# Kernel optimization log

Measured on AMD Instinct MI355X. Metric: run time of the kernel, lower is better.

The kernel has to match this reference:

```python
import jax, jax.numpy as jnp
import numpy as np

EPS = 1e-9
# i = 7,6,...,-1 use exp_factor = -(4**i); i = -2 uses 0.0 (matches torch's reversed(range(-2,8)))
EXP_FACTORS = np.array([-(4.0 ** i) for i in range(7, -2, -1)] + [0.0], dtype=np.float32)


def setup_inputs() -> dict:
    key = jax.random.key(0)
    k1, k2 = jax.random.split(key)
    B, N, D = 16, 2048, 3
    preds = jax.random.normal(k1, (B, N, D), dtype=jnp.float32)
    labels = jax.random.normal(k2, (B, N, D), dtype=jnp.float32)
    return {"preds": preds, "labels": labels}


def _pairwise_dist(p1, p2):
    # ||p1||^2 + ||p2||^2 - 2 p1 . p2  -> [B, N, N]
    p1n = jnp.sum(p1 * p1, axis=-1)[..., :, None]
    p2n = jnp.sum(p2 * p2, axis=-1)[..., None, :]
    return p1n + p2n - 2.0 * jnp.einsum('bnd,bmd->bnm', p1, p2)


def _approx_match(pwdist):
    B, N, _ = pwdist.shape
    match0 = jnp.zeros_like(pwdist)
    cost0 = jnp.ones((B, 1, N), dtype=pwdist.dtype)      # per-target remaining capacity
    curr0 = jnp.ones((B, N, 1), dtype=pwdist.dtype)      # per-source remaining currency

    def step(carry, ef):
        match, cost, currency = carry
        bids = jnp.exp(ef * pwdist) * cost
        bids = bids * currency / (jnp.sum(bids, axis=1, keepdims=True) + EPS)
        bid_wt = jnp.minimum(cost / (jnp.sum(bids, axis=1, keepdims=True) + EPS), 1.0)
        bids = bids * bid_wt
        match = match + bids
        cost = jnp.maximum(cost - jnp.sum(bids, axis=1, keepdims=True), 0.0)
        currency = jnp.maximum(currency - jnp.sum(bids, axis=2, keepdims=True), 0.0)
        return (match, cost, currency), None

    (match, _, _), _ = jax.lax.scan(step, (match0, cost0, curr0), jnp.asarray(EXP_FACTORS))
    return match


def reference(preds, labels):
    pwdist = _pairwise_dist(preds, labels)
    match = _approx_match(pwdist)
    return jnp.sum(match * pwdist)
```

## Files before the change

### kernel.cpp

```cpp
#include <hip/hip_runtime.h>
#include <cstddef>

#define BB    16
#define NN    2048
#define BN    (BB * NN)
#define EPSF  1e-9f
#define TPB   512
#define CPT   2
#define SPLIT 16
#define TILE  128
#define CHUNK 1024

extern "C" __device__ float __ocml_native_exp2_f32(float);
__device__ __forceinline__ float fast_exp2(float x) {
#if __has_builtin(__builtin_amdgcn_exp2f)
    return __builtin_amdgcn_exp2f(x);
#else
    return __ocml_native_exp2_f32(x);
#endif
}

__global__ __launch_bounds__(TPB, 4) void passA(
    const float* __restrict__ preds, const float* __restrict__ labels,
    const float* __restrict__ curprev, float* __restrict__ curout,
    const float* __restrict__ RSprev, const float* __restrict__ RRprev,
    float* __restrict__ RSz, float* __restrict__ RRz,
    float* __restrict__ Sacc, float* __restrict__ Tacc,
    float* __restrict__ out, float c1, int k)
{
    __shared__ float4 s_p[TILE];
    __shared__ float  s_cu[TILE];
    __shared__ float  s_red[2];
    int blk = blockIdx.x;
    int split = blk & 15, mc = (blk >> 4) & 1, b = blk >> 5;
    int t = threadIdx.x;
    int base = b * NN;

    if (t < TILE) {
        int idx = base + split * TILE + t;
        const float* p = preds + (size_t)idx * 3;
        float px = p[0], py = p[1], pz = p[2];
        float pn = px * px + py * py + pz * pz;
        float cu, contrib = 0.0f;
        if (k == 0) cu = 1.0f;
        else {
            float cup = curprev[idx], rs = RSprev[idx], rr = RRprev[idx];
            contrib = cup * rr;
            cu = fmaxf(cup * (1.0f - rs), 0.0f);
        }
        s_p[t]  = make_float4(px, py, pz, c1 * pn);
        s_cu[t] = cu;
        if (mc == 0) {
            curout[idx] = cu;
            RSz[idx] = 0.0f; RRz[idx] = 0.0f;
        }
        if (k > 0 && mc == 0) {
#pragma unroll
            for (int o = 32; o > 0; o >>= 1) contrib += __shfl_down(contrib, o, 64);
            if ((t & 63) == 0) s_red[t >> 6] = contrib;
        }
    }

    int m0 = mc * CHUNK + t;
    float gx[CPT], gy[CPT], gz[CPT], am[CPT], Sa[CPT], Ta[CPT];
    float n2c1 = -2.0f * c1;
#pragma unroll
    for (int c = 0; c < CPT; c++) {
        int m = m0 + c * TPB;
        const float* l = labels + (size_t)(base + m) * 3;
        float lx = l[0], ly = l[1], lz = l[2];
        gx[c] = n2c1 * lx; gy[c] = n2c1 * ly; gz[c] = n2c1 * lz;
        am[c] = c1 * (lx * lx + ly * ly + lz * lz);
        Sa[c] = 0.0f; Ta[c] = 0.0f;
    }
    __syncthreads();
    if (k > 0 && mc == 0 && t == 0) atomicAdd(out, s_red[0] + s_red[1]);

#pragma unroll 8
    for (int j = 0; j < TILE; j++) {
        float4 P = s_p[j]; float cu = s_cu[j];
#pragma unroll
        for (int c = 0; c < CPT; c++) {
            float arg = fmaf(P.x, gx[c], fmaf(P.y, gy[c], fmaf(P.z, gz[c], P.w + am[c])));
            float e = fast_exp2(arg);
            Sa[c] += e;
            Ta[c] = fmaf(e, cu, Ta[c]);
        }
    }
#pragma unroll
    for (int c = 0; c < CPT; c++) {
        int idx = base + m0 + c * TPB;
        atomicAdd(&Sacc[idx], Sa[c]);
        atomicAdd(&Tacc[idx], Ta[c]);
    }
}

__global__ __launch_bounds__(TPB, 4) void passB(
    const float* __restrict__ preds, const float* __restrict__ labels,
    const float* __restrict__ Sread, const float* __restrict__ Tread,
    const float* __restrict__ costprev, float* __restrict__ costout,
    float* __restrict__ Sz, float* __restrict__ Tz,
    float* __restrict__ RSacc, float* __restrict__ RRacc,
    float c1, float invc1, int k, int last)
{
    __shared__ float4 s_l[TILE];
    __shared__ float  s_cc[TILE];
    int blk = blockIdx.x;
    int split = blk & 15, nc = (blk >> 4) & 1, b = blk >> 5;
    int t = threadIdx.x;
    int base = b * NN;

    if (t < TILE) {
        int idx = base + split * TILE + t;
        const float* l = labels + (size_t)idx * 3;
        float lx = l[0], ly = l[1], lz = l[2];
        float lm2 = lx * lx + ly * ly + lz * lz;
        float S = Sread[idx], T = Tread[idx];
        float cost = (k == 0) ? 1.0f : costprev[idx];
        float D1 = fmaf(cost, S, EPSF);
        float S2 = cost * T / D1;
        float bw = fminf(cost / (S2 + EPSF), 1.0f);
        float cc = cost * bw / D1;
        if (nc == 0) {
            costout[idx] = fmaxf(fmaf(-S2, bw, cost), 0.0f);
            Sz[idx] = 0.0f; Tz[idx] = 0.0f;
        }
        if (last) s_l[t] = make_float4(lx, ly, lz, lm2);
        else      s_l[t] = make_float4(-2.0f * c1 * lx, -2.0f * c1 * ly,
                                       -2.0f * c1 * lz, c1 * lm2);
        s_cc[t] = cc;
    }

    int n0 = nc * CHUNK + t;
    float px[CPT], py[CPT], pz[CPT], qq[CPT], RSa[CPT], RRa[CPT];
#pragma unroll
    for (int c = 0; c < CPT; c++) {
        int n = n0 + c * TPB;
        const float* p = preds + (size_t)(base + n) * 3;
        px[c] = p[0]; py[c] = p[1]; pz[c] = p[2];
        float pn = px[c] * px[c] + py[c] * py[c] + pz[c] * pz[c];
        qq[c] = last ? pn : c1 * pn;
        RSa[c] = 0.0f; RRa[c] = 0.0f;
    }
    __syncthreads();

    if (!last) {
#pragma unroll 8
        for (int j = 0; j < TILE; j++) {
            float4 L = s_l[j]; float ccj = s_cc[j];
#pragma unroll
            for (int c = 0; c < CPT; c++) {
                float arg = fmaf(px[c], L.x, fmaf(py[c], L.y, fmaf(pz[c], L.z, qq[c] + L.w)));
                float e = fast_exp2(arg);
                float w = e * ccj;
                RSa[c] += w;
                RRa[c] = fmaf(w, arg, RRa[c]);
            }
        }
#pragma unroll
        for (int c = 0; c < CPT; c++) {
            int idx = base + n0 + c * TPB;
            atomicAdd(&RSacc[idx], RSa[c]);
            atomicAdd(&RRacc[idx], RRa[c] * invc1);
        }
    } else {
#pragma unroll 8
        for (int j = 0; j < TILE; j++) {
            float4 L = s_l[j]; float ccj = s_cc[j];
#pragma unroll
            for (int c = 0; c < CPT; c++) {
                float dot = fmaf(px[c], L.x, fmaf(py[c], L.y, pz[c] * L.z));
                float pw  = fmaf(-2.0f, dot, qq[c] + L.w);
                RRa[c] = fmaf(ccj, pw, RRa[c]);
            }
        }
#pragma unroll
        for (int c = 0; c < CPT; c++) {
            int idx = base + n0 + c * TPB;
            atomicAdd(&RRacc[idx], RRa[c]);
        }
    }
}

__global__ void finalK(const float* __restrict__ cur, const float* __restrict__ RR,
                       float* __restrict__ out)
{
    int t = threadIdx.x;
    int i = blockIdx.x * TPB + t;
    float contrib = cur[i] * RR[i];
#pragma unroll
    for (int o = 32; o > 0; o >>= 1) contrib += __shfl_down(contrib, o, 64);
    __shared__ float s_red[TPB / 64];
    if ((t & 63) == 0) s_red[t >> 6] = contrib;
    __syncthreads();
    if (t == 0) {
        float s = 0.0f;
#pragma unroll
        for (int w = 0; w < TPB / 64; w++) s += s_red[w];
        atomicAdd(out, s);
    }
}

extern "C" void kernel_launch(void* const* d_in, const int* in_sizes, int n_in,
                              void* d_out, int out_size, void* d_ws, size_t ws_size,
                              hipStream_t stream) {
    const float* preds  = (const float*)d_in[0];
    const float* labels = (const float*)d_in[1];
    float* out = (float*)d_out;
    float* ws  = (float*)d_ws;

    float* S[2]     = {ws + 0 * BN, ws + 2 * BN};
    float* T[2]     = {ws + 1 * BN, ws + 3 * BN};
    float* RS[2]    = {ws + 4 * BN, ws + 6 * BN};
    float* RR[2]    = {ws + 5 * BN, ws + 7 * BN};
    float* curb[2]  = {ws + 8 * BN, ws + 9 * BN};
    float* costb[2] = {ws + 10 * BN, ws + 11 * BN};

    hipMemsetAsync(d_out, 0, sizeof(float), stream);
    hipMemsetAsync(ws, 0, (size_t)2 * BN * sizeof(float), stream);

    static const float efs[10] = {-16384.0f, -4096.0f, -1024.0f, -256.0f, -64.0f,
                                  -16.0f, -4.0f, -1.0f, -0.25f, 0.0f};
    const float log2e = 1.44269504088896f;
    for (int k = 0; k < 10; k++) {
        float c1 = efs[k] * log2e;
        float invc1 = (efs[k] != 0.0f) ? 1.0f / c1 : 0.0f;
        int pk = k & 1, pp = (k + 1) & 1;
        passA<<<512, TPB, 0, stream>>>(preds, labels,
            curb[pp], curb[pk],
            RS[pp], RR[pp],
            RS[pk], RR[pk],
            S[pk], T[pk],
            out, c1, k);
        passB<<<512, TPB, 0, stream>>>(preds, labels,
            S[pk], T[pk],
            costb[pk], costb[pp],
            S[pp], T[pp],
            RS[pk], RR[pk],
            c1, invc1, k, (k == 9) ? 1 : 0);
    }
    finalK<<<BN / TPB, TPB, 0, stream>>>(curb[1], RR[1], out);
}
```

Baseline: 350.0 us.

## Collapse final auction step algebraically, skip underflowed exps, retile passes

The last iteration has exp factor zero, so every bid weight is constant. That step is now computed in closed form by a per-batch kernel using moment sums of the labels (count, squared norms, coordinate sums) instead of an N×N pass. For the three sharpest early iterations, wavefront-uniform checks skip exp2 work when every lane's argument is below the float underflow point. Tiling also changes: each block covers all 2048 columns with 4 per thread and 64-row tiles, and the per-row factors are read from shared memory as float4. These are algebraically exact, but the skip relies on exp2 flushing to zero, and the moment-based sum may round differently.

```diff
diff --git a/kernel.cpp b/kernel.cpp
--- a/kernel.cpp
+++ b/kernel.cpp
@@ -6,10 +6,10 @@
 #define BN    (BB * NN)
 #define EPSF  1e-9f
 #define TPB   512
-#define CPT   2
-#define SPLIT 16
-#define TILE  128
-#define CHUNK 1024
+#define CPT   4
+#define SPLIT 32
+#define TILE  64
+#define UFLO  -151.0f
 
 extern "C" __device__ float __ocml_native_exp2_f32(float);
 __device__ __forceinline__ float fast_exp2(float x) {
@@ -20,6 +20,23 @@
 #endif
 }
 
+__device__ __forceinline__ float f4c(float4 v, int u) {
+    return (u == 0) ? v.x : ((u == 1) ? v.y : ((u == 2) ? v.z : v.w));
+}
+
+__device__ __forceinline__ float block_sum(float v, int t, float* tmp8) {
+#pragma unroll
+    for (int o = 32; o > 0; o >>= 1) v += __shfl_down(v, o, 64);
+    __syncthreads();
+    if ((t & 63) == 0) tmp8[t >> 6] = v;
+    __syncthreads();
+    float s = 0.0f;
+#pragma unroll
+    for (int w = 0; w < TPB / 64; w++) s += tmp8[w];
+    return s;
+}
+
+template<int SKIP>
 __global__ __launch_bounds__(TPB, 4) void passA(
     const float* __restrict__ preds, const float* __restrict__ labels,
     const float* __restrict__ curprev, float* __restrict__ curout,
@@ -29,10 +46,10 @@
     float* __restrict__ out, float c1, int k)
 {
     __shared__ float4 s_p[TILE];
-    __shared__ float  s_cu[TILE];
-    __shared__ float  s_red[2];
+    __shared__ float4 s_cu4[TILE / 4];
+    __shared__ float  s_red;
     int blk = blockIdx.x;
-    int split = blk & 15, mc = (blk >> 4) & 1, b = blk >> 5;
+    int split = blk & (SPLIT - 1), b = blk >> 5;
     int t = threadIdx.x;
     int base = b * NN;
 
@@ -48,65 +65,75 @@
             contrib = cup * rr;
             cu = fmaxf(cup * (1.0f - rs), 0.0f);
         }
-        s_p[t]  = make_float4(px, py, pz, c1 * pn);
-        s_cu[t] = cu;
-        if (mc == 0) {
-            curout[idx] = cu;
-            RSz[idx] = 0.0f; RRz[idx] = 0.0f;
-        }
-        if (k > 0 && mc == 0) {
+        s_p[t] = make_float4(px, py, pz, c1 * pn);
+        ((float*)s_cu4)[t] = cu;
+        curout[idx] = cu;
+        RSz[idx] = 0.0f; RRz[idx] = 0.0f;
+        if (k > 0) {
 #pragma unroll
             for (int o = 32; o > 0; o >>= 1) contrib += __shfl_down(contrib, o, 64);
-            if ((t & 63) == 0) s_red[t >> 6] = contrib;
-        }
-    }
-
-    int m0 = mc * CHUNK + t;
+            if (t == 0) s_red = contrib;
+        }
+    }
+
     float gx[CPT], gy[CPT], gz[CPT], am[CPT], Sa[CPT], Ta[CPT];
     float n2c1 = -2.0f * c1;
 #pragma unroll
     for (int c = 0; c < CPT; c++) {
-        int m = m0 + c * TPB;
-        const float* l = labels + (size_t)(base + m) * 3;
+        const float* l = labels + (size_t)(base + t + c * TPB) * 3;
         float lx = l[0], ly = l[1], lz = l[2];
         gx[c] = n2c1 * lx; gy[c] = n2c1 * ly; gz[c] = n2c1 * lz;
         am[c] = c1 * (lx * lx + ly * ly + lz * lz);
         Sa[c] = 0.0f; Ta[c] = 0.0f;
     }
     __syncthreads();
-    if (k > 0 && mc == 0 && t == 0) atomicAdd(out, s_red[0] + s_red[1]);
-
-#pragma unroll 8
-    for (int j = 0; j < TILE; j++) {
-        float4 P = s_p[j]; float cu = s_cu[j];
-#pragma unroll
-        for (int c = 0; c < CPT; c++) {
-            float arg = fmaf(P.x, gx[c], fmaf(P.y, gy[c], fmaf(P.z, gz[c], P.w + am[c])));
-            float e = fast_exp2(arg);
-            Sa[c] += e;
-            Ta[c] = fmaf(e, cu, Ta[c]);
-        }
-    }
-#pragma unroll
-    for (int c = 0; c < CPT; c++) {
-        int idx = base + m0 + c * TPB;
+    if (k > 0 && t == 0) atomicAdd(out, s_red);
+
+#pragma unroll 2
+    for (int j4 = 0; j4 < TILE / 4; j4++) {
+        float4 cu4 = s_cu4[j4];
+#pragma unroll
+        for (int u = 0; u < 4; u++) {
+            float4 P = s_p[j4 * 4 + u];
+            float cu = f4c(cu4, u);
+#pragma unroll
+            for (int c = 0; c < CPT; c++) {
+                float arg = fmaf(P.x, gx[c], fmaf(P.y, gy[c], fmaf(P.z, gz[c], P.w + am[c])));
+                if constexpr (SKIP) {
+                    if (__any(arg > UFLO)) {
+                        float e = fast_exp2(arg);
+                        Sa[c] += e;
+                        Ta[c] = fmaf(e, cu, Ta[c]);
+                    }
+                } else {
+                    float e = fast_exp2(arg);
+                    Sa[c] += e;
+                    Ta[c] = fmaf(e, cu, Ta[c]);
+                }
+            }
+        }
+    }
+#pragma unroll
+    for (int c = 0; c < CPT; c++) {
+        int idx = base + t + c * TPB;
         atomicAdd(&Sacc[idx], Sa[c]);
         atomicAdd(&Tacc[idx], Ta[c]);
     }
 }
 
+template<int SKIP>
 __global__ __launch_bounds__(TPB, 4) void passB(
     const float* __restrict__ preds, const float* __restrict__ labels,
     const float* __restrict__ Sread, const float* __restrict__ Tread,
     const float* __restrict__ costprev, float* __restrict__ costout,
     float* __restrict__ Sz, float* __restrict__ Tz,
     float* __restrict__ RSacc, float* __restrict__ RRacc,
-    float c1, float invc1, int k, int last)
+    float c1, float invc1, int k)
 {
     __shared__ float4 s_l[TILE];
-    __shared__ float  s_cc[TILE];
+    __shared__ float4 s_cc4[TILE / 4];
     int blk = blockIdx.x;
-    int split = blk & 15, nc = (blk >> 4) & 1, b = blk >> 5;
+    int split = blk & (SPLIT - 1), b = blk >> 5;
     int t = threadIdx.x;
     int base = b * NN;
 
@@ -121,84 +148,113 @@
         float S2 = cost * T / D1;
         float bw = fminf(cost / (S2 + EPSF), 1.0f);
         float cc = cost * bw / D1;
-        if (nc == 0) {
-            costout[idx] = fmaxf(fmaf(-S2, bw, cost), 0.0f);
-            Sz[idx] = 0.0f; Tz[idx] = 0.0f;
-        }
-        if (last) s_l[t] = make_float4(lx, ly, lz, lm2);
-        else      s_l[t] = make_float4(-2.0f * c1 * lx, -2.0f * c1 * ly,
-                                       -2.0f * c1 * lz, c1 * lm2);
-        s_cc[t] = cc;
-    }
-
-    int n0 = nc * CHUNK + t;
+        costout[idx] = fmaxf(fmaf(-S2, bw, cost), 0.0f);
+        Sz[idx] = 0.0f; Tz[idx] = 0.0f;
+        s_l[t] = make_float4(-2.0f * c1 * lx, -2.0f * c1 * ly,
+                             -2.0f * c1 * lz, c1 * lm2);
+        ((float*)s_cc4)[t] = cc;
+    }
+
     float px[CPT], py[CPT], pz[CPT], qq[CPT], RSa[CPT], RRa[CPT];
 #pragma unroll
     for (int c = 0; c < CPT; c++) {
-        int n = n0 + c * TPB;
-        const float* p = preds + (size_t)(base + n) * 3;
+        const float* p = preds + (size_t)(base + t + c * TPB) * 3;
         px[c] = p[0]; py[c] = p[1]; pz[c] = p[2];
-        float pn = px[c] * px[c] + py[c] * py[c] + pz[c] * pz[c];
-        qq[c] = last ? pn : c1 * pn;
+        qq[c] = c1 * (px[c] * px[c] + py[c] * py[c] + pz[c] * pz[c]);
         RSa[c] = 0.0f; RRa[c] = 0.0f;
     }
     __syncthreads();
 
-    if (!last) {
-#pragma unroll 8
-        for (int j = 0; j < TILE; j++) {
-            float4 L = s_l[j]; float ccj = s_cc[j];
+#pragma unroll 2
+    for (int j4 = 0; j4 < TILE / 4; j4++) {
+        float4 cc4 = s_cc4[j4];
+#pragma unroll
+        for (int u = 0; u < 4; u++) {
+            float4 L = s_l[j4 * 4 + u];
+            float ccj = f4c(cc4, u);
 #pragma unroll
             for (int c = 0; c < CPT; c++) {
                 float arg = fmaf(px[c], L.x, fmaf(py[c], L.y, fmaf(pz[c], L.z, qq[c] + L.w)));
-                float e = fast_exp2(arg);
-                float w = e * ccj;
-                RSa[c] += w;
-                RRa[c] = fmaf(w, arg, RRa[c]);
+                if constexpr (SKIP) {
+                    if (__any(arg > UFLO)) {
+                        float e = fast_exp2(arg);
+                        float w = e * ccj;
+                        RSa[c] += w;
+                        RRa[c] = fmaf(w, arg, RRa[c]);
+                    }
+                } else {
+                    float e = fast_exp2(arg);
+                    float w = e * ccj;
+                    RSa[c] += w;
+                    RRa[c] = fmaf(w, arg, RRa[c]);
+                }
             }
         }
-#pragma unroll
-        for (int c = 0; c < CPT; c++) {
-            int idx = base + n0 + c * TPB;
-            atomicAdd(&RSacc[idx], RSa[c]);
-            atomicAdd(&RRacc[idx], RRa[c] * invc1);
-        }
-    } else {
-#pragma unroll 8
-        for (int j = 0; j < TILE; j++) {
-            float4 L = s_l[j]; float ccj = s_cc[j];
-#pragma unroll
-            for (int c = 0; c < CPT; c++) {
-                float dot = fmaf(px[c], L.x, fmaf(py[c], L.y, pz[c] * L.z));
-                float pw  = fmaf(-2.0f, dot, qq[c] + L.w);
-                RRa[c] = fmaf(ccj, pw, RRa[c]);
-            }
-        }
-#pragma unroll
-        for (int c = 0; c < CPT; c++) {
-            int idx = base + n0 + c * TPB;
-            atomicAdd(&RRacc[idx], RRa[c]);
-        }
-    }
-}
-
-__global__ void finalK(const float* __restrict__ cur, const float* __restrict__ RR,
-                       float* __restrict__ out)
+    }
+#pragma unroll
+    for (int c = 0; c < CPT; c++) {
+        int idx = base + t + c * TPB;
+        atomicAdd(&RSacc[idx], RSa[c]);
+        atomicAdd(&RRacc[idx], RRa[c] * invc1);
+    }
+}
+
+__global__ __launch_bounds__(TPB, 1) void k9(
+    const float* __restrict__ preds, const float* __restrict__ labels,
+    const float* __restrict__ cur8, const float* __restrict__ RS8,
+    const float* __restrict__ RR8, const float* __restrict__ cost9,
+    float* __restrict__ out)
 {
-    int t = threadIdx.x;
-    int i = blockIdx.x * TPB + t;
-    float contrib = cur[i] * RR[i];
-#pragma unroll
-    for (int o = 32; o > 0; o >>= 1) contrib += __shfl_down(contrib, o, 64);
-    __shared__ float s_red[TPB / 64];
-    if ((t & 63) == 0) s_red[t >> 6] = contrib;
-    __syncthreads();
-    if (t == 0) {
-        float s = 0.0f;
-#pragma unroll
-        for (int w = 0; w < TPB / 64; w++) s += s_red[w];
-        atomicAdd(out, s);
-    }
+    __shared__ float tmp8[TPB / 64];
+    int b = blockIdx.x, t = threadIdx.x;
+    int base = b * NN;
+
+    float cu9[CPT];
+    float contrib = 0.0f, csum = 0.0f;
+#pragma unroll
+    for (int c = 0; c < CPT; c++) {
+        int idx = base + t + c * TPB;
+        float cup = cur8[idx];
+        contrib = fmaf(cup, RR8[idx], contrib);
+        float cu = fmaxf(cup * (1.0f - RS8[idx]), 0.0f);
+        cu9[c] = cu; csum += cu;
+    }
+    float contribT = block_sum(contrib, t, tmp8);
+    float Cb = block_sum(csum, t, tmp8);
+
+    float A = 0.0f, Bs = 0.0f, Vx = 0.0f, Vy = 0.0f, Vz = 0.0f;
+#pragma unroll
+    for (int c = 0; c < CPT; c++) {
+        int idx = base + t + c * TPB;
+        const float* l = labels + (size_t)idx * 3;
+        float lx = l[0], ly = l[1], lz = l[2];
+        float cost = cost9[idx];
+        float D1 = fmaf(cost, 2048.0f, EPSF);
+        float S2 = cost * Cb / D1;
+        float bw = fminf(cost / (S2 + EPSF), 1.0f);
+        float cc = cost * bw / D1;
+        A += cc;
+        Bs = fmaf(cc, lx * lx + ly * ly + lz * lz, Bs);
+        Vx = fmaf(cc, lx, Vx); Vy = fmaf(cc, ly, Vy); Vz = fmaf(cc, lz, Vz);
+    }
+    float At  = block_sum(A, t, tmp8);
+    float Bt  = block_sum(Bs, t, tmp8);
+    float Vxt = block_sum(Vx, t, tmp8);
+    float Vyt = block_sum(Vy, t, tmp8);
+    float Vzt = block_sum(Vz, t, tmp8);
+
+    float acc = 0.0f;
+#pragma unroll
+    for (int c = 0; c < CPT; c++) {
+        int idx = base + t + c * TPB;
+        const float* p = preds + (size_t)idx * 3;
+        float x = p[0], y = p[1], z = p[2];
+        float pn = x * x + y * y + z * z;
+        float rr = fmaf(At, pn, Bt) - 2.0f * (x * Vxt + y * Vyt + z * Vzt);
+        acc = fmaf(cu9[c], rr, acc);
+    }
+    float accT = block_sum(acc, t, tmp8);
+    if (t == 0) atomicAdd(out, contribT + accT);
 }
 
 extern "C" void kernel_launch(void* const* d_in, const int* in_sizes, int n_in,
@@ -219,25 +275,28 @@
     hipMemsetAsync(d_out, 0, sizeof(float), stream);
     hipMemsetAsync(ws, 0, (size_t)2 * BN * sizeof(float), stream);
 
-    static const float efs[10] = {-16384.0f, -4096.0f, -1024.0f, -256.0f, -64.0f,
-                                  -16.0f, -4.0f, -1.0f, -0.25f, 0.0f};
+    static const float efs[9] = {-16384.0f, -4096.0f, -1024.0f, -256.0f, -64.0f,
+                                 -16.0f, -4.0f, -1.0f, -0.25f};
     const float log2e = 1.44269504088896f;
-    for (int k = 0; k < 10; k++) {
+    for (int k = 0; k < 9; k++) {
         float c1 = efs[k] * log2e;
-        float invc1 = (efs[k] != 0.0f) ? 1.0f / c1 : 0.0f;
+        float invc1 = 1.0f / c1;
         int pk = k & 1, pp = (k + 1) & 1;
-        passA<<<512, TPB, 0, stream>>>(preds, labels,
-            curb[pp], curb[pk],
-            RS[pp], RR[pp],
-            RS[pk], RR[pk],
-            S[pk], T[pk],
-            out, c1, k);
-        passB<<<512, TPB, 0, stream>>>(preds, labels,
-            S[pk], T[pk],
-            costb[pk], costb[pp],
-            S[pp], T[pp],
-            RS[pk], RR[pk],
-            c1, invc1, k, (k == 9) ? 1 : 0);
-    }
-    finalK<<<BN / TPB, TPB, 0, stream>>>(curb[1], RR[1], out);
-}
+        if (k <= 2) {
+            passA<1><<<512, TPB, 0, stream>>>(preds, labels,
+                curb[pp], curb[pk], RS[pp], RR[pp], RS[pk], RR[pk],
+                S[pk], T[pk], out, c1, k);
+            passB<1><<<512, TPB, 0, stream>>>(preds, labels,
+                S[pk], T[pk], costb[pk], costb[pp], S[pp], T[pp],
+                RS[pk], RR[pk], c1, invc1, k);
+        } else {
+            passA<0><<<512, TPB, 0, stream>>>(preds, labels,
+                curb[pp], curb[pk], RS[pp], RR[pp], RS[pk], RR[pk],
+                S[pk], T[pk], out, c1, k);
+            passB<0><<<512, TPB, 0, stream>>>(preds, labels,
+                S[pk], T[pk], costb[pk], costb[pp], S[pp], T[pp],
+                RS[pk], RR[pk], c1, invc1, k);
+        }
+    }
+    k9<<<BB, TPB, 0, stream>>>(preds, labels, curb[0], RS[0], RR[0], costb[1], out);
+}
```

Result: slower. 376.1 us (+7.5%).

## Solve zero-factor final iteration in closed form and pack pair math into v_pk ops

Applied to the files above, without the earlier changes.

With exp factor zero every bid weight is one, so the last iteration's pairwise pass collapses to per-batch moment sums: total weight, a weighted norm sum and a weighted centroid of the labels. A single per-batch kernel now computes it in O(N) instead of O(N^2), replacing the final passA/passB pair and finalK. The inner loops of passA and passB are also rewritten to process two tile entries at once with packed FP32 instructions (v_pk_fma/add/mul) over a split shared-memory layout. The risks are a serialized 16-block kernel and precision differences from the moment-based expansion.

```diff
diff --git a/kernel.cpp b/kernel.cpp
--- a/kernel.cpp
+++ b/kernel.cpp
@@ -10,6 +10,10 @@
 #define SPLIT 16
 #define TILE  128
 #define CHUNK 1024
+#define K9C   4
+
+typedef float v2f __attribute__((ext_vector_type(2)));
+typedef float v4f __attribute__((ext_vector_type(4)));
 
 extern "C" __device__ float __ocml_native_exp2_f32(float);
 __device__ __forceinline__ float fast_exp2(float x) {
@@ -18,6 +22,34 @@
 #else
     return __ocml_native_exp2_f32(x);
 #endif
+}
+
+__device__ __forceinline__ v2f pk_fma(v2f a, v2f b, v2f c) {
+    v2f d;
+    asm("v_pk_fma_f32 %0, %1, %2, %3" : "=v"(d) : "v"(a), "v"(b), "v"(c));
+    return d;
+}
+__device__ __forceinline__ v2f pk_add(v2f a, v2f b) {
+    v2f d;
+    asm("v_pk_add_f32 %0, %1, %2" : "=v"(d) : "v"(a), "v"(b));
+    return d;
+}
+__device__ __forceinline__ v2f pk_mul(v2f a, v2f b) {
+    v2f d;
+    asm("v_pk_mul_f32 %0, %1, %2" : "=v"(d) : "v"(a), "v"(b));
+    return d;
+}
+
+__device__ __forceinline__ float block_sum(float v, int t, float* tmp8) {
+#pragma unroll
+    for (int o = 32; o > 0; o >>= 1) v += __shfl_down(v, o, 64);
+    __syncthreads();
+    if ((t & 63) == 0) tmp8[t >> 6] = v;
+    __syncthreads();
+    float s = 0.0f;
+#pragma unroll
+    for (int w = 0; w < TPB / 64; w++) s += tmp8[w];
+    return s;
 }
 
 __global__ __launch_bounds__(TPB, 4) void passA(
@@ -28,9 +60,10 @@
     float* __restrict__ Sacc, float* __restrict__ Tacc,
     float* __restrict__ out, float c1, int k)
 {
-    __shared__ float4 s_p[TILE];
-    __shared__ float  s_cu[TILE];
-    __shared__ float  s_red[2];
+    __shared__ v4f s_pa[TILE / 2];
+    __shared__ v4f s_pb[TILE / 2];
+    __shared__ v2f s_cu2[TILE / 2];
+    __shared__ float s_red[2];
     int blk = blockIdx.x;
     int split = blk & 15, mc = (blk >> 4) & 1, b = blk >> 5;
     int t = threadIdx.x;
@@ -48,8 +81,12 @@
             contrib = cup * rr;
             cu = fmaxf(cup * (1.0f - rs), 0.0f);
         }
-        s_p[t]  = make_float4(px, py, pz, c1 * pn);
-        s_cu[t] = cu;
+        int h = t >> 1, par = t & 1;
+        float* pa = (float*)&s_pa[h];
+        float* pb = (float*)&s_pb[h];
+        pa[par] = px; pa[2 + par] = py;
+        pb[par] = pz; pb[2 + par] = c1 * pn;
+        ((float*)s_cu2)[t] = cu;
         if (mc == 0) {
             curout[idx] = cu;
             RSz[idx] = 0.0f; RRz[idx] = 0.0f;
@@ -62,36 +99,45 @@
     }
 
     int m0 = mc * CHUNK + t;
-    float gx[CPT], gy[CPT], gz[CPT], am[CPT], Sa[CPT], Ta[CPT];
+    v2f gx2[CPT], gy2[CPT], gz2[CPT], am2[CPT], Sa2[CPT], Ta2[CPT];
     float n2c1 = -2.0f * c1;
 #pragma unroll
     for (int c = 0; c < CPT; c++) {
         int m = m0 + c * TPB;
         const float* l = labels + (size_t)(base + m) * 3;
         float lx = l[0], ly = l[1], lz = l[2];
-        gx[c] = n2c1 * lx; gy[c] = n2c1 * ly; gz[c] = n2c1 * lz;
-        am[c] = c1 * (lx * lx + ly * ly + lz * lz);
-        Sa[c] = 0.0f; Ta[c] = 0.0f;
+        float gx = n2c1 * lx, gy = n2c1 * ly, gz = n2c1 * lz;
+        float am = c1 * (lx * lx + ly * ly + lz * lz);
+        gx2[c] = (v2f){gx, gx}; gy2[c] = (v2f){gy, gy}; gz2[c] = (v2f){gz, gz};
+        am2[c] = (v2f){am, am};
+        Sa2[c] = (v2f){0.0f, 0.0f}; Ta2[c] = (v2f){0.0f, 0.0f};
     }
     __syncthreads();
     if (k > 0 && mc == 0 && t == 0) atomicAdd(out, s_red[0] + s_red[1]);
 
-#pragma unroll 8
-    for (int j = 0; j < TILE; j++) {
-        float4 P = s_p[j]; float cu = s_cu[j];
+#pragma unroll 4
+    for (int h = 0; h < TILE / 2; h++) {
+        v4f A1 = s_pa[h];
+        v4f A2 = s_pb[h];
+        v2f cu2 = s_cu2[h];
 #pragma unroll
         for (int c = 0; c < CPT; c++) {
-            float arg = fmaf(P.x, gx[c], fmaf(P.y, gy[c], fmaf(P.z, gz[c], P.w + am[c])));
-            float e = fast_exp2(arg);
-            Sa[c] += e;
-            Ta[c] = fmaf(e, cu, Ta[c]);
+            v2f seed = pk_add(A2.zw, am2[c]);
+            v2f arg = pk_fma(A1.xy, gx2[c],
+                      pk_fma(A1.zw, gy2[c],
+                      pk_fma(A2.xy, gz2[c], seed)));
+            v2f e2;
+            e2.x = fast_exp2(arg.x);
+            e2.y = fast_exp2(arg.y);
+            Sa2[c] = pk_add(Sa2[c], e2);
+            Ta2[c] = pk_fma(e2, cu2, Ta2[c]);
         }
     }
 #pragma unroll
     for (int c = 0; c < CPT; c++) {
         int idx = base + m0 + c * TPB;
-        atomicAdd(&Sacc[idx], Sa[c]);
-        atomicAdd(&Tacc[idx], Ta[c]);
+        atomicAdd(&Sacc[idx], Sa2[c].x + Sa2[c].y);
+        atomicAdd(&Tacc[idx], Ta2[c].x + Ta2[c].y);
     }
 }
 
@@ -101,10 +147,11 @@
     const float* __restrict__ costprev, float* __restrict__ costout,
     float* __restrict__ Sz, float* __restrict__ Tz,
     float* __restrict__ RSacc, float* __restrict__ RRacc,
-    float c1, float invc1, int k, int last)
+    float c1, float invc1, int k)
 {
-    __shared__ float4 s_l[TILE];
-    __shared__ float  s_cc[TILE];
+    __shared__ v4f s_la[TILE / 2];
+    __shared__ v4f s_lb[TILE / 2];
+    __shared__ v2f s_cc2[TILE / 2];
     int blk = blockIdx.x;
     int split = blk & 15, nc = (blk >> 4) & 1, b = blk >> 5;
     int t = threadIdx.x;
@@ -121,84 +168,116 @@
         float S2 = cost * T / D1;
         float bw = fminf(cost / (S2 + EPSF), 1.0f);
         float cc = cost * bw / D1;
+        int h = t >> 1, par = t & 1;
+        float* la = (float*)&s_la[h];
+        float* lb = (float*)&s_lb[h];
+        float n2c1 = -2.0f * c1;
+        la[par] = n2c1 * lx; la[2 + par] = n2c1 * ly;
+        lb[par] = n2c1 * lz; lb[2 + par] = c1 * lm2;
+        ((float*)s_cc2)[t] = cc;
         if (nc == 0) {
             costout[idx] = fmaxf(fmaf(-S2, bw, cost), 0.0f);
             Sz[idx] = 0.0f; Tz[idx] = 0.0f;
         }
-        if (last) s_l[t] = make_float4(lx, ly, lz, lm2);
-        else      s_l[t] = make_float4(-2.0f * c1 * lx, -2.0f * c1 * ly,
-                                       -2.0f * c1 * lz, c1 * lm2);
-        s_cc[t] = cc;
     }
 
     int n0 = nc * CHUNK + t;
-    float px[CPT], py[CPT], pz[CPT], qq[CPT], RSa[CPT], RRa[CPT];
+    v2f px2[CPT], py2[CPT], pz2[CPT], qq2[CPT], RSa2[CPT], RRa2[CPT];
 #pragma unroll
     for (int c = 0; c < CPT; c++) {
         int n = n0 + c * TPB;
         const float* p = preds + (size_t)(base + n) * 3;
-        px[c] = p[0]; py[c] = p[1]; pz[c] = p[2];
-        float pn = px[c] * px[c] + py[c] * py[c] + pz[c] * pz[c];
-        qq[c] = last ? pn : c1 * pn;
-        RSa[c] = 0.0f; RRa[c] = 0.0f;
+        float px = p[0], py = p[1], pz = p[2];
+        float qq = c1 * (px * px + py * py + pz * pz);
+        px2[c] = (v2f){px, px}; py2[c] = (v2f){py, py}; pz2[c] = (v2f){pz, pz};
+        qq2[c] = (v2f){qq, qq};
+        RSa2[c] = (v2f){0.0f, 0.0f}; RRa2[c] = (v2f){0.0f, 0.0f};
     }
     __syncthreads();
 
-    if (!last) {
-#pragma unroll 8
-        for (int j = 0; j < TILE; j++) {
-            float4 L = s_l[j]; float ccj = s_cc[j];
-#pragma unroll
-            for (int c = 0; c < CPT; c++) {
-                float arg = fmaf(px[c], L.x, fmaf(py[c], L.y, fmaf(pz[c], L.z, qq[c] + L.w)));
-                float e = fast_exp2(arg);
-                float w = e * ccj;
-                RSa[c] += w;
-                RRa[c] = fmaf(w, arg, RRa[c]);
-            }
-        }
+#pragma unroll 4
+    for (int h = 0; h < TILE / 2; h++) {
+        v4f L1 = s_la[h];
+        v4f L2 = s_lb[h];
+        v2f cc2 = s_cc2[h];
 #pragma unroll
         for (int c = 0; c < CPT; c++) {
-            int idx = base + n0 + c * TPB;
-            atomicAdd(&RSacc[idx], RSa[c]);
-            atomicAdd(&RRacc[idx], RRa[c] * invc1);
-        }
-    } else {
-#pragma unroll 8
-        for (int j = 0; j < TILE; j++) {
-            float4 L = s_l[j]; float ccj = s_cc[j];
-#pragma unroll
-            for (int c = 0; c < CPT; c++) {
-                float dot = fmaf(px[c], L.x, fmaf(py[c], L.y, pz[c] * L.z));
-                float pw  = fmaf(-2.0f, dot, qq[c] + L.w);
-                RRa[c] = fmaf(ccj, pw, RRa[c]);
-            }
-        }
-#pragma unroll
-        for (int c = 0; c < CPT; c++) {
-            int idx = base + n0 + c * TPB;
-            atomicAdd(&RRacc[idx], RRa[c]);
-        }
-    }
-}
-
-__global__ void finalK(const float* __restrict__ cur, const float* __restrict__ RR,
-                       float* __restrict__ out)
+            v2f seed = pk_add(L2.zw, qq2[c]);
+            v2f arg = pk_fma(L1.xy, px2[c],
+                      pk_fma(L1.zw, py2[c],
+                      pk_fma(L2.xy, pz2[c], seed)));
+            v2f e2;
+            e2.x = fast_exp2(arg.x);
+            e2.y = fast_exp2(arg.y);
+            v2f w2 = pk_mul(e2, cc2);
+            RSa2[c] = pk_add(RSa2[c], w2);
+            RRa2[c] = pk_fma(w2, arg, RRa2[c]);
+        }
+    }
+#pragma unroll
+    for (int c = 0; c < CPT; c++) {
+        int idx = base + n0 + c * TPB;
+        atomicAdd(&RSacc[idx], RSa2[c].x + RSa2[c].y);
+        atomicAdd(&RRacc[idx], (RRa2[c].x + RRa2[c].y) * invc1);
+    }
+}
+
+__global__ __launch_bounds__(TPB, 1) void k9(
+    const float* __restrict__ preds, const float* __restrict__ labels,
+    const float* __restrict__ cur8, const float* __restrict__ RS8,
+    const float* __restrict__ RR8, const float* __restrict__ cost9,
+    float* __restrict__ out)
 {
-    int t = threadIdx.x;
-    int i = blockIdx.x * TPB + t;
-    float contrib = cur[i] * RR[i];
-#pragma unroll
-    for (int o = 32; o > 0; o >>= 1) contrib += __shfl_down(contrib, o, 64);
-    __shared__ float s_red[TPB / 64];
-    if ((t & 63) == 0) s_red[t >> 6] = contrib;
-    __syncthreads();
-    if (t == 0) {
-        float s = 0.0f;
-#pragma unroll
-        for (int w = 0; w < TPB / 64; w++) s += s_red[w];
-        atomicAdd(out, s);
-    }
+    __shared__ float tmp8[TPB / 64];
+    int b = blockIdx.x, t = threadIdx.x;
+    int base = b * NN;
+
+    float cu9[K9C];
+    float contrib = 0.0f, csum = 0.0f;
+#pragma unroll
+    for (int c = 0; c < K9C; c++) {
+        int idx = base + t + c * TPB;
+        float cup = cur8[idx];
+        contrib = fmaf(cup, RR8[idx], contrib);
+        float cu = fmaxf(cup * (1.0f - RS8[idx]), 0.0f);
+        cu9[c] = cu; csum += cu;
+    }
+    float contribT = block_sum(contrib, t, tmp8);
+    float Cb = block_sum(csum, t, tmp8);
+
+    float A = 0.0f, Bs = 0.0f, Vx = 0.0f, Vy = 0.0f, Vz = 0.0f;
+#pragma unroll
+    for (int c = 0; c < K9C; c++) {
+        int idx = base + t + c * TPB;
+        const float* l = labels + (size_t)idx * 3;
+        float lx = l[0], ly = l[1], lz = l[2];
+        float cost = cost9[idx];
+        float D1 = fmaf(cost, 2048.0f, EPSF);
+        float S2 = cost * Cb / D1;
+        float bw = fminf(cost / (S2 + EPSF), 1.0f);
+        float cc = cost * bw / D1;
+        A += cc;
+        Bs = fmaf(cc, lx * lx + ly * ly + lz * lz, Bs);
+        Vx = fmaf(cc, lx, Vx); Vy = fmaf(cc, ly, Vy); Vz = fmaf(cc, lz, Vz);
+    }
+    float At  = block_sum(A, t, tmp8);
+    float Bt  = block_sum(Bs, t, tmp8);
+    float Vxt = block_sum(Vx, t, tmp8);
+    float Vyt = block_sum(Vy, t, tmp8);
+    float Vzt = block_sum(Vz, t, tmp8);
+
+    float acc = 0.0f;
+#pragma unroll
+    for (int c = 0; c < K9C; c++) {
+        int idx = base + t + c * TPB;
+        const float* p = preds + (size_t)idx * 3;
+        float x = p[0], y = p[1], z = p[2];
+        float pn = x * x + y * y + z * z;
+        float rr = fmaf(At, pn, Bt) - 2.0f * (x * Vxt + y * Vyt + z * Vzt);
+        acc = fmaf(cu9[c], rr, acc);
+    }
+    float accT = block_sum(acc, t, tmp8);
+    if (t == 0) atomicAdd(out, contribT + accT);
 }
 
 extern "C" void kernel_launch(void* const* d_in, const int* in_sizes, int n_in,
@@ -219,12 +298,12 @@
     hipMemsetAsync(d_out, 0, sizeof(float), stream);
     hipMemsetAsync(ws, 0, (size_t)2 * BN * sizeof(float), stream);
 
-    static const float efs[10] = {-16384.0f, -4096.0f, -1024.0f, -256.0f, -64.0f,
-                                  -16.0f, -4.0f, -1.0f, -0.25f, 0.0f};
+    static const float efs[9] = {-16384.0f, -4096.0f, -1024.0f, -256.0f, -64.0f,
+                                 -16.0f, -4.0f, -1.0f, -0.25f};
     const float log2e = 1.44269504088896f;
-    for (int k = 0; k < 10; k++) {
+    for (int k = 0; k < 9; k++) {
         float c1 = efs[k] * log2e;
-        float invc1 = (efs[k] != 0.0f) ? 1.0f / c1 : 0.0f;
+        float invc1 = 1.0f / c1;
         int pk = k & 1, pp = (k + 1) & 1;
         passA<<<512, TPB, 0, stream>>>(preds, labels,
             curb[pp], curb[pk],
@@ -237,7 +316,7 @@
             costb[pk], costb[pp],
             S[pp], T[pp],
             RS[pk], RR[pk],
-            c1, invc1, k, (k == 9) ? 1 : 0);
-    }
-    finalK<<<BN / TPB, TPB, 0, stream>>>(curb[1], RR[1], out);
-}
+            c1, invc1, k);
+    }
+    k9<<<BB, TPB, 0, stream>>>(preds, labels, curb[0], RS[0], RR[0], costb[1], out);
+}
```

Result: faster. 308.8 us, median of 2 (-11.8%).
